# Kernel optimization log

Hardware: AMD Instinct MI355X
Metric: run time of the kernel (lower is better)

## Reference

```python
import jax, jax.numpy as jnp
import numpy as np

N = 500_000
B = 8192
D = 128
EPS = 1e-5


def setup_inputs() -> dict:
    key = jax.random.key(0)
    ks = jax.random.split(key, 8)
    h = jax.random.normal(ks[0], (N, D), dtype=jnp.float32)
    batch = jnp.sort(jax.random.randint(ks[1], (N,), 0, B)).astype(jnp.int64)
    vn_h = jax.random.normal(ks[2], (B, D), dtype=jnp.float32)
    # layer 0 MLP params: Linear(D,D) -> LayerNorm(D) -> ReLU -> Linear(D,D)
    W1 = jax.random.normal(ks[3], (D, D), dtype=jnp.float32) * 0.02
    b1 = jnp.zeros((D,), dtype=jnp.float32)
    ln_g = jnp.ones((D,), dtype=jnp.float32)
    ln_b = jnp.zeros((D,), dtype=jnp.float32)
    W2 = jax.random.normal(ks[4], (D, D), dtype=jnp.float32) * 0.02
    b2 = jnp.zeros((D,), dtype=jnp.float32)
    return {"h": h, "batch": batch, "vn_h": vn_h, "W1": W1, "b1": b1,
            "ln_g": ln_g, "ln_b": ln_b, "W2": W2, "b2": b2}


def _layernorm(x, g, b):
    mu = jnp.mean(x, axis=-1, keepdims=True)
    var = jnp.mean(jnp.square(x - mu), axis=-1, keepdims=True)
    return (x - mu) * jax.lax.rsqrt(var + EPS) * g + b


def reference(h, batch, vn_h, W1, b1, ln_g, ln_b, W2, b2):
    batch = batch.astype(jnp.int32)
    # global_mean_pool: segment mean of node features per graph  [B, D]
    seg_sum = jax.ops.segment_sum(h, batch, num_segments=B)
    counts = jax.ops.segment_sum(jnp.ones((h.shape[0],), h.dtype), batch, num_segments=B)
    pooled = seg_sum / jnp.maximum(counts, 1.0)[:, None]
    vn_h_new = pooled + vn_h
    # vn MLP: Linear -> LayerNorm -> ReLU -> Linear
    x = vn_h_new @ W1.T + b1
    x = jax.nn.relu(_layernorm(x, ln_g, ln_b))
    vn_out = x @ W2.T + b2                      # [B, D]
    h_out = h + vn_out[batch]                   # broadcast gather back to nodes
    return h_out, vn_out
```

## Files before the change

kernel.cpp:

```cpp
#include <hip/hip_runtime.h>

#define DIM 128
#define EPS 1e-5f

typedef short           bf16x8 __attribute__((ext_vector_type(8)));
typedef unsigned short  u16x4  __attribute__((ext_vector_type(4)));
typedef float           f32x4  __attribute__((ext_vector_type(4)));

__device__ __forceinline__ unsigned short f2b(float f) {
    unsigned int u = __builtin_bit_cast(unsigned int, f);
    unsigned int r = (u + 0x7FFFu + ((u >> 16) & 1u)) >> 16;
    return (unsigned short)r;
}
__device__ __forceinline__ bf16x8 ldw8(const float* __restrict__ p) {
    f32x4 a = *reinterpret_cast<const f32x4*>(p);
    f32x4 b = *reinterpret_cast<const f32x4*>(p + 4);
    bf16x8 r;
    #pragma unroll
    for (int j = 0; j < 4; ++j) {
        r[j]     = (short)f2b(a[j]);
        r[j + 4] = (short)f2b(b[j]);
    }
    return r;
}

__global__ __launch_bounds__(256) void k_pool_mlp(
    const float* __restrict__ h, const int* __restrict__ batch,
    const float* __restrict__ vn,
    const float* __restrict__ W1, const float* __restrict__ b1,
    const float* __restrict__ lng, const float* __restrict__ lnb,
    const float* __restrict__ W2, const float* __restrict__ b2v,
    float* __restrict__ vn_out, int n_nodes)
{
    __shared__ int sb[17];
    __shared__ unsigned short xtile[16][136];

    const int tid = threadIdx.x;
    const int G0  = blockIdx.x * 16;

    if (tid < 17) {
        const int target = G0 + tid;
        int lo = 0, hi = n_nodes;
        while (lo < hi) {
            int mid = (lo + hi) >> 1;
            if (batch[mid] < target) lo = mid + 1; else hi = mid;
        }
        sb[tid] = lo;
    }
    __syncthreads();

    const int gi = tid >> 4;
    const int j  = tid & 15;
    const int s = sb[gi], e = sb[gi + 1];

    f32x4 a0 = (f32x4){0.f, 0.f, 0.f, 0.f};
    f32x4 a1 = (f32x4){0.f, 0.f, 0.f, 0.f};
    for (int n = s; n < e; ++n) {
        const float* p = h + (size_t)n * DIM + j * 4;
        a0 += *reinterpret_cast<const f32x4*>(p);
        a1 += *reinterpret_cast<const f32x4*>(p + 64);
    }

    const int cnt = e - s;
    const float inv = 1.0f / (float)(cnt > 1 ? cnt : 1);
    const float* vp = vn + (size_t)(G0 + gi) * DIM + j * 4;
    f32x4 v0 = *reinterpret_cast<const f32x4*>(vp);
    f32x4 v1 = *reinterpret_cast<const f32x4*>(vp + 64);
    u16x4 x0, x1;
    #pragma unroll
    for (int q = 0; q < 4; ++q) {
        x0[q] = f2b(fmaf(a0[q], inv, v0[q]));
        x1[q] = f2b(fmaf(a1[q], inv, v1[q]));
    }
    *reinterpret_cast<u16x4*>(&xtile[gi][j * 4])      = x0;
    *reinterpret_cast<u16x4*>(&xtile[gi][j * 4 + 64]) = x1;
    __syncthreads();

    if (tid < 64) {
        const int lane  = tid;
        const int row16 = lane & 15;
        const int kgrp  = lane >> 4;

        bf16x8 afrag[4];
        #pragma unroll
        for (int kk = 0; kk < 4; ++kk)
            afrag[kk] = *reinterpret_cast<const bf16x8*>(&xtile[row16][kgrp * 8 + kk * 32]);

        f32x4 acc[8];
        #pragma unroll
        for (int t = 0; t < 8; ++t) acc[t] = (f32x4){0.f, 0.f, 0.f, 0.f};
        #pragma unroll
        for (int t = 0; t < 8; ++t) {
            const float* wp = W1 + (size_t)(t * 16 + row16) * DIM + kgrp * 8;
            #pragma unroll
            for (int kk = 0; kk < 4; ++kk) {
                bf16x8 bfrag = ldw8(wp + kk * 32);
                acc[t] = __builtin_amdgcn_mfma_f32_16x16x32_bf16(afrag[kk], bfrag, acc[t], 0, 0, 0);
            }
        }

        float b1f[8], gf[8], bf_[8], b2f8[8];
        #pragma unroll
        for (int t = 0; t < 8; ++t) {
            const int f = t * 16 + row16;
            b1f[t]  = b1[f];
            gf[t]   = lng[f];
            bf_[t]  = lnb[f];
            b2f8[t] = b2v[f];
        }
        #pragma unroll
        for (int t = 0; t < 8; ++t)
            #pragma unroll
            for (int r = 0; r < 4; ++r) acc[t][r] += b1f[t];

        #pragma unroll
        for (int r = 0; r < 4; ++r) {
            float sm = 0.f, ss = 0.f;
            #pragma unroll
            for (int t = 0; t < 8; ++t) { sm += acc[t][r]; ss += acc[t][r] * acc[t][r]; }
            #pragma unroll
            for (int m = 1; m <= 8; m <<= 1) {
                sm += __shfl_xor(sm, m);
                ss += __shfl_xor(ss, m);
            }
            const float mu  = sm * (1.0f / 128.0f);
            const float var = ss * (1.0f / 128.0f) - mu * mu;
            const float rs  = rsqrtf(var + EPS);
            const int   gm  = kgrp * 4 + r;
            #pragma unroll
            for (int t = 0; t < 8; ++t) {
                float z = (acc[t][r] - mu) * rs * gf[t] + bf_[t];
                z = fmaxf(z, 0.f);
                xtile[gm][t * 16 + row16] = f2b(z);
            }
        }

        bf16x8 afrag2[4];
        #pragma unroll
        for (int kk = 0; kk < 4; ++kk)
            afrag2[kk] = *reinterpret_cast<const bf16x8*>(&xtile[row16][kgrp * 8 + kk * 32]);

        f32x4 acc2[8];
        #pragma unroll
        for (int t = 0; t < 8; ++t) acc2[t] = (f32x4){0.f, 0.f, 0.f, 0.f};
        #pragma unroll
        for (int t = 0; t < 8; ++t) {
            const float* wp = W2 + (size_t)(t * 16 + row16) * DIM + kgrp * 8;
            #pragma unroll
            for (int kk = 0; kk < 4; ++kk) {
                bf16x8 bfrag = ldw8(wp + kk * 32);
                acc2[t] = __builtin_amdgcn_mfma_f32_16x16x32_bf16(afrag2[kk], bfrag, acc2[t], 0, 0, 0);
            }
        }

        #pragma unroll
        for (int r = 0; r < 4; ++r) {
            float* op = vn_out + (size_t)(G0 + kgrp * 4 + r) * DIM + row16;
            #pragma unroll
            for (int t = 0; t < 8; ++t)
                op[t * 16] = acc2[t][r] + b2f8[t];
        }
    }
}

__global__ __launch_bounds__(256) void k_add(
    const float* __restrict__ h, const int* __restrict__ batch,
    const float* __restrict__ vn_out, float* __restrict__ h_out,
    int n_nodes)
{
    const long total = (long)n_nodes * 16;
    for (long u = (long)blockIdx.x * blockDim.x + threadIdx.x; u < total;
         u += (long)gridDim.x * blockDim.x) {
        const int n = (int)(u >> 4);
        const int c = ((int)u & 15) * 8;
        const float* hp = h + (size_t)n * DIM + c;
        f32x4 h0 = *reinterpret_cast<const f32x4*>(hp);
        f32x4 h1 = *reinterpret_cast<const f32x4*>(hp + 4);
        const int b = batch[n];
        const float* vp = vn_out + (size_t)b * DIM + c;
        f32x4 v0 = *reinterpret_cast<const f32x4*>(vp);
        f32x4 v1 = *reinterpret_cast<const f32x4*>(vp + 4);
        float* op = h_out + (size_t)n * DIM + c;
        __builtin_nontemporal_store(h0 + v0, reinterpret_cast<f32x4*>(op));
        __builtin_nontemporal_store(h1 + v1, reinterpret_cast<f32x4*>(op + 4));
    }
}

extern "C" void kernel_launch(void* const* d_in, const int* in_sizes, int n_in,
                              void* d_out, int out_size, void* d_ws, size_t ws_size,
                              hipStream_t stream)
{
    const float* h    = (const float*)d_in[0];
    const int*   bat  = (const int*)d_in[1];
    const float* vn   = (const float*)d_in[2];
    const float* W1   = (const float*)d_in[3];
    const float* b1   = (const float*)d_in[4];
    const float* lng  = (const float*)d_in[5];
    const float* lnb  = (const float*)d_in[6];
    const float* W2   = (const float*)d_in[7];
    const float* b2v  = (const float*)d_in[8];

    const int n_nodes = in_sizes[0] / DIM;
    const int nb      = in_sizes[2] / DIM;

    float* out    = (float*)d_out;
    float* h_out  = out;
    float* vn_out = out + (size_t)n_nodes * DIM;

    k_pool_mlp<<<nb / 16, 256, 0, stream>>>(h, bat, vn, W1, b1, lng, lnb,
                                            W2, b2v, vn_out, n_nodes);
    k_add<<<2048, 256, 0, stream>>>(h, bat, vn_out, h_out, n_nodes);
}
```

Baseline: 154.9 us.

## Fuse broadcast-add into pool+MLP kernel, reusing segment bounds per graph

Merges the node broadcast-add pass into the pooling/MLP kernel. Each block keeps its 16 graphs' MLP outputs in shared memory and re-reads its own contiguous node ranges to write h + vn_out, so the separate kernel launch and the per-node batch index gather go away. The second pass over h may also hit in L2 right after pooling. In exchange, the add work is limited to only 512 blocks, each handling a serial per-graph loop over about 61 nodes, which may cap memory parallelism. Per-thread column mapping also changes to 8 contiguous floats.

```diff
diff --git a/kernel.cpp b/kernel.cpp
--- a/kernel.cpp
+++ b/kernel.cpp
@@ -4,7 +4,7 @@
 #define EPS 1e-5f
 
 typedef short           bf16x8 __attribute__((ext_vector_type(8)));
-typedef unsigned short  u16x4  __attribute__((ext_vector_type(4)));
+typedef unsigned short  u16x8  __attribute__((ext_vector_type(8)));
 typedef float           f32x4  __attribute__((ext_vector_type(4)));
 
 __device__ __forceinline__ unsigned short f2b(float f) {
@@ -24,16 +24,17 @@
     return r;
 }
 
-__global__ __launch_bounds__(256) void k_pool_mlp(
+__global__ __launch_bounds__(256) void k_fused(
     const float* __restrict__ h, const int* __restrict__ batch,
     const float* __restrict__ vn,
     const float* __restrict__ W1, const float* __restrict__ b1,
     const float* __restrict__ lng, const float* __restrict__ lnb,
     const float* __restrict__ W2, const float* __restrict__ b2v,
-    float* __restrict__ vn_out, int n_nodes)
+    float* __restrict__ vn_out, float* __restrict__ h_out, int n_nodes)
 {
     __shared__ int sb[17];
     __shared__ unsigned short xtile[16][136];
+    __shared__ float vtile[16][132];
 
     const int tid = threadIdx.x;
     const int G0  = blockIdx.x * 16;
@@ -56,24 +57,22 @@
     f32x4 a0 = (f32x4){0.f, 0.f, 0.f, 0.f};
     f32x4 a1 = (f32x4){0.f, 0.f, 0.f, 0.f};
     for (int n = s; n < e; ++n) {
-        const float* p = h + (size_t)n * DIM + j * 4;
+        const float* p = h + (size_t)n * DIM + j * 8;
         a0 += *reinterpret_cast<const f32x4*>(p);
-        a1 += *reinterpret_cast<const f32x4*>(p + 64);
-    }
-
+        a1 += *reinterpret_cast<const f32x4*>(p + 4);
+    }
     const int cnt = e - s;
     const float inv = 1.0f / (float)(cnt > 1 ? cnt : 1);
-    const float* vp = vn + (size_t)(G0 + gi) * DIM + j * 4;
+    const float* vp = vn + (size_t)(G0 + gi) * DIM + j * 8;
     f32x4 v0 = *reinterpret_cast<const f32x4*>(vp);
-    f32x4 v1 = *reinterpret_cast<const f32x4*>(vp + 64);
-    u16x4 x0, x1;
+    f32x4 v1 = *reinterpret_cast<const f32x4*>(vp + 4);
+    u16x8 xv;
     #pragma unroll
     for (int q = 0; q < 4; ++q) {
-        x0[q] = f2b(fmaf(a0[q], inv, v0[q]));
-        x1[q] = f2b(fmaf(a1[q], inv, v1[q]));
-    }
-    *reinterpret_cast<u16x4*>(&xtile[gi][j * 4])      = x0;
-    *reinterpret_cast<u16x4*>(&xtile[gi][j * 4 + 64]) = x1;
+        xv[q]     = f2b(fmaf(a0[q], inv, v0[q]));
+        xv[q + 4] = f2b(fmaf(a1[q], inv, v1[q]));
+    }
+    *reinterpret_cast<u16x8*>(&xtile[gi][j * 8]) = xv;
     __syncthreads();
 
     if (tid < 64) {
@@ -155,34 +154,30 @@
 
         #pragma unroll
         for (int r = 0; r < 4; ++r) {
-            float* op = vn_out + (size_t)(G0 + kgrp * 4 + r) * DIM + row16;
+            const int gm = kgrp * 4 + r;
             #pragma unroll
             for (int t = 0; t < 8; ++t)
-                op[t * 16] = acc2[t][r] + b2f8[t];
-        }
-    }
-}
-
-__global__ __launch_bounds__(256) void k_add(
-    const float* __restrict__ h, const int* __restrict__ batch,
-    const float* __restrict__ vn_out, float* __restrict__ h_out,
-    int n_nodes)
-{
-    const long total = (long)n_nodes * 16;
-    for (long u = (long)blockIdx.x * blockDim.x + threadIdx.x; u < total;
-         u += (long)gridDim.x * blockDim.x) {
-        const int n = (int)(u >> 4);
-        const int c = ((int)u & 15) * 8;
-        const float* hp = h + (size_t)n * DIM + c;
-        f32x4 h0 = *reinterpret_cast<const f32x4*>(hp);
-        f32x4 h1 = *reinterpret_cast<const f32x4*>(hp + 4);
-        const int b = batch[n];
-        const float* vp = vn_out + (size_t)b * DIM + c;
-        f32x4 v0 = *reinterpret_cast<const f32x4*>(vp);
-        f32x4 v1 = *reinterpret_cast<const f32x4*>(vp + 4);
-        float* op = h_out + (size_t)n * DIM + c;
-        __builtin_nontemporal_store(h0 + v0, reinterpret_cast<f32x4*>(op));
-        __builtin_nontemporal_store(h1 + v1, reinterpret_cast<f32x4*>(op + 4));
+                vtile[gm][t * 16 + row16] = acc2[t][r] + b2f8[t];
+        }
+    }
+    __syncthreads();
+
+    {
+        const float* src = &vtile[gi][j * 8];
+        float* dst = vn_out + (size_t)(G0 + gi) * DIM + j * 8;
+        *reinterpret_cast<f32x4*>(dst)     = *reinterpret_cast<const f32x4*>(src);
+        *reinterpret_cast<f32x4*>(dst + 4) = *reinterpret_cast<const f32x4*>(src + 4);
+    }
+
+    f32x4 w0 = *reinterpret_cast<const f32x4*>(&vtile[gi][j * 8]);
+    f32x4 w1 = *reinterpret_cast<const f32x4*>(&vtile[gi][j * 8 + 4]);
+    for (int n = s; n < e; ++n) {
+        const float* p = h + (size_t)n * DIM + j * 8;
+        f32x4 h0 = *reinterpret_cast<const f32x4*>(p);
+        f32x4 h1 = *reinterpret_cast<const f32x4*>(p + 4);
+        float* op = h_out + (size_t)n * DIM + j * 8;
+        __builtin_nontemporal_store(h0 + w0, reinterpret_cast<f32x4*>(op));
+        __builtin_nontemporal_store(h1 + w1, reinterpret_cast<f32x4*>(op + 4));
     }
 }
 
@@ -207,7 +202,6 @@
     float* h_out  = out;
     float* vn_out = out + (size_t)n_nodes * DIM;
 
-    k_pool_mlp<<<nb / 16, 256, 0, stream>>>(h, bat, vn, W1, b1, lng, lnb,
-                                            W2, b2v, vn_out, n_nodes);
-    k_add<<<2048, 256, 0, stream>>>(h, bat, vn_out, h_out, n_nodes);
-}
+    k_fused<<<nb / 16, 256, 0, stream>>>(h, bat, vn, W1, b1, lng, lnb,
+                                         W2, b2v, vn_out, h_out, n_nodes);
+}
```

Measured after the change: 149.7 us. 3.4% less time.

## Precompute segment bounds, vectorize pool loads, reverse add loop order for L2 reuse

Applied to the files above, without the earlier changes.

Adds a small kernel that writes segment start offsets from the sorted batch array, replacing the per-block binary searches in the pooling kernel. The pooling threads now read 8 contiguous floats each and store one 16-byte bf16 vector to shared memory. The add kernel walks its grid-stride loop in reverse so that the tail of h, likely still in L2 from the pooling pass, is read first. The trade is an extra kernel launch and reliance on the workspace buffer.

```diff
diff --git a/kernel.cpp b/kernel.cpp
--- a/kernel.cpp
+++ b/kernel.cpp
@@ -4,7 +4,7 @@
 #define EPS 1e-5f
 
 typedef short           bf16x8 __attribute__((ext_vector_type(8)));
-typedef unsigned short  u16x4  __attribute__((ext_vector_type(4)));
+typedef unsigned short  u16x8  __attribute__((ext_vector_type(8)));
 typedef float           f32x4  __attribute__((ext_vector_type(4)));
 
 __device__ __forceinline__ unsigned short f2b(float f) {
@@ -24,8 +24,18 @@
     return r;
 }
 
+__global__ __launch_bounds__(256) void k_bounds(
+    const int* __restrict__ batch, int* __restrict__ bounds, int n_nodes, int nb)
+{
+    const int idx = blockIdx.x * blockDim.x + threadIdx.x;
+    if (idx > n_nodes) return;
+    const int cur  = (idx < n_nodes) ? batch[idx] : nb;
+    const int prev = (idx > 0) ? batch[idx - 1] : -1;
+    for (int b = prev + 1; b <= cur; ++b) bounds[b] = idx;
+}
+
 __global__ __launch_bounds__(256) void k_pool_mlp(
-    const float* __restrict__ h, const int* __restrict__ batch,
+    const float* __restrict__ h, const int* __restrict__ bounds,
     const float* __restrict__ vn,
     const float* __restrict__ W1, const float* __restrict__ b1,
     const float* __restrict__ lng, const float* __restrict__ lnb,
@@ -38,15 +48,7 @@
     const int tid = threadIdx.x;
     const int G0  = blockIdx.x * 16;
 
-    if (tid < 17) {
-        const int target = G0 + tid;
-        int lo = 0, hi = n_nodes;
-        while (lo < hi) {
-            int mid = (lo + hi) >> 1;
-            if (batch[mid] < target) lo = mid + 1; else hi = mid;
-        }
-        sb[tid] = lo;
-    }
+    if (tid < 17) sb[tid] = bounds[G0 + tid];
     __syncthreads();
 
     const int gi = tid >> 4;
@@ -56,30 +58,27 @@
     f32x4 a0 = (f32x4){0.f, 0.f, 0.f, 0.f};
     f32x4 a1 = (f32x4){0.f, 0.f, 0.f, 0.f};
     for (int n = s; n < e; ++n) {
-        const float* p = h + (size_t)n * DIM + j * 4;
+        const float* p = h + (size_t)n * DIM + j * 8;
         a0 += *reinterpret_cast<const f32x4*>(p);
-        a1 += *reinterpret_cast<const f32x4*>(p + 64);
-    }
-
+        a1 += *reinterpret_cast<const f32x4*>(p + 4);
+    }
     const int cnt = e - s;
     const float inv = 1.0f / (float)(cnt > 1 ? cnt : 1);
-    const float* vp = vn + (size_t)(G0 + gi) * DIM + j * 4;
+    const float* vp = vn + (size_t)(G0 + gi) * DIM + j * 8;
     f32x4 v0 = *reinterpret_cast<const f32x4*>(vp);
-    f32x4 v1 = *reinterpret_cast<const f32x4*>(vp + 64);
-    u16x4 x0, x1;
+    f32x4 v1 = *reinterpret_cast<const f32x4*>(vp + 4);
+    u16x8 xv;
     #pragma unroll
     for (int q = 0; q < 4; ++q) {
-        x0[q] = f2b(fmaf(a0[q], inv, v0[q]));
-        x1[q] = f2b(fmaf(a1[q], inv, v1[q]));
-    }
-    *reinterpret_cast<u16x4*>(&xtile[gi][j * 4])      = x0;
-    *reinterpret_cast<u16x4*>(&xtile[gi][j * 4 + 64]) = x1;
+        xv[q]     = f2b(fmaf(a0[q], inv, v0[q]));
+        xv[q + 4] = f2b(fmaf(a1[q], inv, v1[q]));
+    }
+    *reinterpret_cast<u16x8*>(&xtile[gi][j * 8]) = xv;
     __syncthreads();
 
     if (tid < 64) {
-        const int lane  = tid;
-        const int row16 = lane & 15;
-        const int kgrp  = lane >> 4;
+        const int row16 = tid & 15;
+        const int kgrp  = tid >> 4;
 
         bf16x8 afrag[4];
         #pragma unroll
@@ -169,8 +168,11 @@
     int n_nodes)
 {
     const long total = (long)n_nodes * 16;
-    for (long u = (long)blockIdx.x * blockDim.x + threadIdx.x; u < total;
-         u += (long)gridDim.x * blockDim.x) {
+    const long GS    = (long)gridDim.x * blockDim.x;
+    const long gtid  = (long)blockIdx.x * blockDim.x + threadIdx.x;
+    for (long base = ((total + GS - 1) / GS - 1) * GS; base >= 0; base -= GS) {
+        const long u = base + gtid;
+        if (u >= total) continue;
         const int n = (int)(u >> 4);
         const int c = ((int)u & 15) * 8;
         const float* hp = h + (size_t)n * DIM + c;
@@ -206,8 +208,10 @@
     float* out    = (float*)d_out;
     float* h_out  = out;
     float* vn_out = out + (size_t)n_nodes * DIM;
-
-    k_pool_mlp<<<nb / 16, 256, 0, stream>>>(h, bat, vn, W1, b1, lng, lnb,
+    int*   bounds = (int*)d_ws;
+
+    k_bounds<<<(n_nodes + 256) / 256, 256, 0, stream>>>(bat, bounds, n_nodes, nb);
+    k_pool_mlp<<<nb / 16, 256, 0, stream>>>(h, bounds, vn, W1, b1, lng, lnb,
                                             W2, b2v, vn_out, n_nodes);
     k_add<<<2048, 256, 0, stream>>>(h, bat, vn_out, h_out, n_nodes);
 }
```

New measurement: 156.0 us. Within noise of the previous version (+0.7%).
